# Optimization experiments

Measured on AMD Instinct MI355X. Metric: run time of the kernel, lower is better.

Reference implementation:

```python
import jax, jax.numpy as jnp
import numpy as np

H = 16        # num_heads
NB = 64       # n_buckets
NH = 6        # n_hyperplanes = log2(NB)


def setup_inputs() -> dict:
    key = jax.random.key(0)
    k = jax.random.split(key, 6)
    E = 1024
    B, S = 2, 2048
    return {
        "x": jax.random.normal(k[0], (B, S, E), jnp.float32),
        "Wq": jax.random.normal(k[1], (E, E), jnp.float32) * (E ** -0.5),
        "bq": jax.random.normal(k[2], (E,), jnp.float32) * 0.02,
        "Wv": jax.random.normal(k[3], (E, E), jnp.float32) * (E ** -0.5),
        "bv": jax.random.normal(k[4], (E,), jnp.float32) * 0.02,
        "hyperplanes": jax.random.normal(k[5], (E // H + 1, NH), jnp.float32),
    }


def reference(x, Wq, bq, Wv, bv, hyperplanes):
    B, S, E = x.shape
    Dh = E // H
    # projections (torch Linear: x @ W.T + b)
    q = (x @ Wq.T + bq).reshape(B, S, H, Dh)
    v = (x @ Wv.T + bv).reshape(B, S, H, Dh)

    # LSH buckets from q: append a ones column, sign-project onto hyperplanes
    qa = jnp.concatenate([q, jnp.ones((B, S, H, 1), q.dtype)], axis=-1)  # [B,S,H,Dh+1]
    proj = jnp.einsum('bshe,en->bshn', qa, hyperplanes)
    bits = (proj >= 0).astype(jnp.int32)
    buckets = jnp.einsum('bshn,n->bsh', bits, 2 ** jnp.arange(NH, dtype=jnp.int32))  # [B,S,H]
    b_hs = buckets.transpose(0, 2, 1)  # [B,H,S]

    q = q.transpose(0, 2, 1, 3)  # [B,H,S,Dh]
    v = v.transpose(0, 2, 1, 3)

    # The original sums, over all NB buckets i, of (q with bucket-i tokens zeroed)
    # times its transpose. Closed form of that sum:
    #   sum_i (1-d[bs,i])(1-d[bt,i]) = NB - 2 + [bs == bt]
    scores = jnp.einsum('bhsd,bhtd->bhst', q, q) / jnp.sqrt(jnp.float32(E))
    same = (b_hs[:, :, :, None] == b_hs[:, :, None, :]).astype(scores.dtype)
    coeff = (NB - 2) + same
    attn = jax.nn.softmax(scores * coeff, axis=-1)  # [B,H,S,S]

    out = jnp.einsum('bhst,bhtd->bhsd', attn, v)
    return out.transpose(0, 2, 1, 3).reshape(B, S, E)
```

## Files before the change

### kernel.cpp

```cpp
#include <hip/hip_runtime.h>


typedef short short8 __attribute__((ext_vector_type(8)));
typedef float f32x4 __attribute__((ext_vector_type(4)));
typedef unsigned short us4 __attribute__((ext_vector_type(4)));

__device__ __forceinline__ float bff(unsigned short h) {
    return __uint_as_float(((unsigned int)h) << 16);
}
__device__ __forceinline__ unsigned short f2bf(float f) {
    unsigned int u = __float_as_uint(f);
    u += 0x7fffu + ((u >> 16) & 1u);
    return (unsigned short)(u >> 16);
}

__device__ __forceinline__ void glds16(const unsigned short* g, unsigned short* l) {
    __builtin_amdgcn_global_load_lds(
        (const __attribute__((address_space(1))) unsigned int*)g,
        (__attribute__((address_space(3))) unsigned int*)l, 16, 0, 0);
}

__global__ __launch_bounds__(256) void split_kernel(
    const float* __restrict__ in, unsigned short* __restrict__ hi,
    unsigned short* __restrict__ lo, int n4)
{
    const int idx = blockIdx.x * 256 + threadIdx.x;
    if (idx >= n4) return;
    const float4 v = ((const float4*)in)[idx];
    us4 h;
    h.x = f2bf(v.x); h.y = f2bf(v.y); h.z = f2bf(v.z); h.w = f2bf(v.w);
    ((us4*)hi)[idx] = h;
    if (lo) {
        us4 l;
        l.x = f2bf(v.x - bff(h.x)); l.y = f2bf(v.y - bff(h.y));
        l.z = f2bf(v.z - bff(h.z)); l.w = f2bf(v.w - bff(h.w));
        ((us4*)lo)[idx] = l;
    }
}

__global__ __launch_bounds__(256, 1) void gemm_q(
    const unsigned short* __restrict__ xh, const unsigned short* __restrict__ xl,
    const unsigned short* __restrict__ wh, const unsigned short* __restrict__ wl,
    const float* __restrict__ bias, float* __restrict__ Qf,
    unsigned short* __restrict__ Qb, unsigned short* __restrict__ Qlo)
{
    __shared__ unsigned short Ah[128 * 64], Al[128 * 64];
    __shared__ unsigned short Bh[128 * 64], Bl[128 * 64];

    const int tid = threadIdx.x;
    const int w = tid >> 6, lane = tid & 63;
    const int i = lane & 15, qd = lane >> 4;
    const int l8 = lane >> 3, j = lane & 7;
    const int m0 = blockIdx.x * 128;
    const int n0 = blockIdx.y * 128;
    const int nw = w * 32;

    f32x4 acc[8][2];
#pragma unroll
    for (int a = 0; a < 8; ++a)
#pragma unroll
        for (int b2 = 0; b2 < 2; ++b2) acc[a][b2] = f32x4{0.f, 0.f, 0.f, 0.f};

    for (int k0 = 0; k0 < 1024; k0 += 64) {
        __syncthreads();
        const int gro = ((j ^ l8) << 3);
#pragma unroll
        for (int c = 0; c < 4; ++c) {
            const int r = w * 32 + c * 8;
            const size_t gx = (size_t)(m0 + r + l8) * 1024 + k0 + gro;
            const size_t gw = (size_t)(n0 + r + l8) * 1024 + k0 + gro;
            glds16(xh + gx, &Ah[r * 64]);
            glds16(xl + gx, &Al[r * 64]);
            glds16(wh + gw, &Bh[r * 64]);
            glds16(wl + gw, &Bl[r * 64]);
        }
        __syncthreads();

#pragma unroll
        for (int kc = 0; kc < 2; ++kc) {
            const int ch = (((kc * 4 + qd) ^ (i & 7)) << 3);
            short8 ah[8], al[8], bh2[2], bl2[2];
#pragma unroll
            for (int mm = 0; mm < 8; ++mm) {
                ah[mm] = *(const short8*)&Ah[(mm * 16 + i) * 64 + ch];
                al[mm] = *(const short8*)&Al[(mm * 16 + i) * 64 + ch];
            }
#pragma unroll
            for (int nn = 0; nn < 2; ++nn) {
                bh2[nn] = *(const short8*)&Bh[(nw + nn * 16 + i) * 64 + ch];
                bl2[nn] = *(const short8*)&Bl[(nw + nn * 16 + i) * 64 + ch];
            }
#pragma unroll
            for (int mm = 0; mm < 8; ++mm)
#pragma unroll
                for (int nn = 0; nn < 2; ++nn) {
                    acc[mm][nn] = __builtin_amdgcn_mfma_f32_16x16x32_bf16(
                        ah[mm], bh2[nn], acc[mm][nn], 0, 0, 0);
                    acc[mm][nn] = __builtin_amdgcn_mfma_f32_16x16x32_bf16(
                        al[mm], bh2[nn], acc[mm][nn], 0, 0, 0);
                    acc[mm][nn] = __builtin_amdgcn_mfma_f32_16x16x32_bf16(
                        ah[mm], bl2[nn], acc[mm][nn], 0, 0, 0);
                }
        }
    }

#pragma unroll
    for (int mm = 0; mm < 8; ++mm)
#pragma unroll
        for (int nn = 0; nn < 2; ++nn)
#pragma unroll
            for (int rr = 0; rr < 4; ++rr) {
                const int row = m0 + mm * 16 + qd * 4 + rr;
                const int col = n0 + nw + nn * 16 + i;
                const float v = acc[mm][nn][rr] + bias[col];
                Qf[(size_t)row * 1024 + col] = v;
                const unsigned short hs = f2bf(v);
                const float lo = v - bff(hs);
                const int b = row >> 11, s = row & 2047;
                const int hh = col >> 6, d = col & 63;
                const size_t oi = ((size_t)((b << 4) + hh) * 2048 + s) * 64 + d;
                Qb[oi] = hs;
                Qlo[oi] = f2bf(lo);
            }
}

__global__ __launch_bounds__(256, 1) void gemm_v(
    const unsigned short* __restrict__ wh, const unsigned short* __restrict__ xh,
    const float* __restrict__ bias, unsigned short* __restrict__ Vt)
{
    __shared__ unsigned short Ah[128 * 64];
    __shared__ unsigned short Bh[128 * 64];

    const int tid = threadIdx.x;
    const int w = tid >> 6, lane = tid & 63;
    const int i = lane & 15, qd = lane >> 4;
    const int l8 = lane >> 3, j = lane & 7;
    const int m0 = blockIdx.x * 128;
    const int n0 = blockIdx.y * 128;
    const int nw = w * 32;

    f32x4 acc[8][2];
#pragma unroll
    for (int a = 0; a < 8; ++a)
#pragma unroll
        for (int b2 = 0; b2 < 2; ++b2) acc[a][b2] = f32x4{0.f, 0.f, 0.f, 0.f};

    for (int k0 = 0; k0 < 1024; k0 += 64) {
        __syncthreads();
        const int gro = ((j ^ l8) << 3);
#pragma unroll
        for (int c = 0; c < 4; ++c) {
            const int r = w * 32 + c * 8;
            glds16(wh + (size_t)(m0 + r + l8) * 1024 + k0 + gro, &Ah[r * 64]);
            glds16(xh + (size_t)(n0 + r + l8) * 1024 + k0 + gro, &Bh[r * 64]);
        }
        __syncthreads();

#pragma unroll
        for (int kc = 0; kc < 2; ++kc) {
            const int ch = (((kc * 4 + qd) ^ (i & 7)) << 3);
            short8 af[8], bf2[2];
#pragma unroll
            for (int mm = 0; mm < 8; ++mm)
                af[mm] = *(const short8*)&Ah[(mm * 16 + i) * 64 + ch];
#pragma unroll
            for (int nn = 0; nn < 2; ++nn)
                bf2[nn] = *(const short8*)&Bh[(nw + nn * 16 + i) * 64 + ch];
#pragma unroll
            for (int mm = 0; mm < 8; ++mm)
#pragma unroll
                for (int nn = 0; nn < 2; ++nn)
                    acc[mm][nn] = __builtin_amdgcn_mfma_f32_16x16x32_bf16(
                        af[mm], bf2[nn], acc[mm][nn], 0, 0, 0);
        }
    }

#pragma unroll
    for (int mm = 0; mm < 8; ++mm)
#pragma unroll
        for (int nn = 0; nn < 2; ++nn)
#pragma unroll
            for (int rr = 0; rr < 4; ++rr) {
                const int rch = m0 + mm * 16 + qd * 4 + rr;
                const int tok = n0 + nw + nn * 16 + i;
                const float v = acc[mm][nn][rr] + bias[rch];
                const int b = tok >> 11, s = tok & 2047;
                Vt[((size_t)(b * 1024 + rch)) * 2048 + s] = f2bf(v);
            }
}

__global__ __launch_bounds__(256) void bucket_kernel(
    const float* __restrict__ Qf, const float* __restrict__ hp,
    int* __restrict__ buckets, float* __restrict__ rown)
{
    __shared__ float hpl[65 * 6];
    const int tid = threadIdx.x;
    if (tid < 65 * 6) hpl[tid] = hp[tid];
    __syncthreads();

    const int idx = blockIdx.x * 256 + tid;
    const int m = idx >> 4, h = idx & 15;
    const float* qrow = Qf + (size_t)m * 1024 + h * 64;

    float pj[6];
    float nrm = 0.f;
#pragma unroll
    for (int n = 0; n < 6; ++n) pj[n] = hpl[64 * 6 + n];
    for (int d = 0; d < 64; ++d) {
        const float qv = qrow[d];
        nrm = fmaf(qv, qv, nrm);
#pragma unroll
        for (int n = 0; n < 6; ++n) pj[n] = fmaf(qv, hpl[d * 6 + n], pj[n]);
    }
    int bkt = 0;
#pragma unroll
    for (int n = 0; n < 6; ++n) bkt |= (pj[n] >= 0.f) << n;
    const int off = ((m >> 11) * 16 + h) * 2048 + (m & 2047);
    buckets[off] = bkt;
    rown[off] = nrm;
}

__global__ __launch_bounds__(256, 2) void attn_kernel(
    const unsigned short* __restrict__ Qb, const unsigned short* __restrict__ Qlo,
    const unsigned short* __restrict__ Vt, const int* __restrict__ bks,
    const float* __restrict__ rown, float* __restrict__ out)
{
    __shared__ unsigned short Khi[64 * 64];
    __shared__ unsigned short Klo[64 * 64];
    __shared__ unsigned short Vs[64 * 64];
    __shared__ unsigned short P[4][2][16 * 64];
    __shared__ float smax[4];

    const int tid = threadIdx.x;
    const int w = tid >> 6, lane = tid & 63;
    const int i = lane & 15, qd = lane >> 4;
    const int l8 = lane >> 3, j = lane & 7;
    const int bh = blockIdx.x;
    const int qbase = blockIdx.y * 128 + w * 32;

    const unsigned short* Qh = Qb + (size_t)bh * 2048 * 64;
    const unsigned short* Ql = Qlo + (size_t)bh * 2048 * 64;
    const unsigned short* Vb = Vt + (size_t)bh * 64 * 2048;
    const int* bk = bks + bh * 2048;
    const float* rnh = rown + bh * 2048;

    float lm = 0.f;
    for (int t = tid; t < 2048; t += 256) lm = fmaxf(lm, rnh[t]);
#pragma unroll
    for (int msk = 1; msk < 64; msk <<= 1) lm = fmaxf(lm, __shfl_xor(lm, msk));
    if (lane == 0) smax[w] = lm;
    __syncthreads();
    const float sqM = sqrtf(fmaxf(fmaxf(smax[0], smax[1]),
                                  fmaxf(smax[2], smax[3])));

    float mrow[2][4], lrun[2][4];
    int qbr[2][4];
#pragma unroll
    for (int ms = 0; ms < 2; ++ms)
#pragma unroll
        for (int r = 0; r < 4; ++r) {
            const int row = qbase + ms * 16 + qd * 4 + r;
            mrow[ms][r] = 1.96875f * sqrtf(rnh[row]) * sqM + 0.5f;
            qbr[ms][r] = bk[row];
            lrun[ms][r] = 0.f;
        }

    short8 aqh0[2], aqh1[2], aql0[2], aql1[2];
#pragma unroll
    for (int ms = 0; ms < 2; ++ms) {
        const unsigned short* qp = Qh + (size_t)(qbase + ms * 16 + i) * 64 + qd * 8;
        const unsigned short* lp = Ql + (size_t)(qbase + ms * 16 + i) * 64 + qd * 8;
        aqh0[ms] = *(const short8*)qp; aqh1[ms] = *(const short8*)(qp + 32);
        aql0[ms] = *(const short8*)lp; aql1[ms] = *(const short8*)(lp + 32);
    }

    f32x4 o[2][4];
#pragma unroll
    for (int ms = 0; ms < 2; ++ms)
#pragma unroll
        for (int d = 0; d < 4; ++d) o[ms][d] = f32x4{0.f, 0.f, 0.f, 0.f};

    for (int t0 = 0; t0 < 2048; t0 += 64) {
        __syncthreads();
#pragma unroll
        for (int c2 = 0; c2 < 2; ++c2) {
            const int r = w * 16 + c2 * 8 + l8;
            const int swz = ((j ^ l8) << 3);
            glds16(Qh + (size_t)(t0 + r) * 64 + swz, &Khi[w * 1024 + c2 * 512]);
            glds16(Ql + (size_t)(t0 + r) * 64 + swz, &Klo[w * 1024 + c2 * 512]);
            glds16(Vb + (size_t)r * 2048 + t0 + swz, &Vs[w * 1024 + c2 * 512]);
        }
        __syncthreads();

        f32x4 s[2][4];
        int kb[4];
#pragma unroll
        for (int sub = 0; sub < 4; ++sub) {
            const int kr = sub * 16 + i;
            const int sw = i & 7;
            const short8 bh0 = *(const short8*)&Khi[kr * 64 + ((qd ^ sw) << 3)];
            const short8 bh1 = *(const short8*)&Khi[kr * 64 + (((qd + 4) ^ sw) << 3)];
            const short8 bl0 = *(const short8*)&Klo[kr * 64 + ((qd ^ sw) << 3)];
            const short8 bl1 = *(const short8*)&Klo[kr * 64 + (((qd + 4) ^ sw) << 3)];
            kb[sub] = bk[t0 + kr];
#pragma unroll
            for (int ms = 0; ms < 2; ++ms) {
                f32x4 t = f32x4{0.f, 0.f, 0.f, 0.f};
                t = __builtin_amdgcn_mfma_f32_16x16x32_bf16(aqh0[ms], bh0, t, 0, 0, 0);
                t = __builtin_amdgcn_mfma_f32_16x16x32_bf16(aqh1[ms], bh1, t, 0, 0, 0);
                t = __builtin_amdgcn_mfma_f32_16x16x32_bf16(aql0[ms], bh0, t, 0, 0, 0);
                t = __builtin_amdgcn_mfma_f32_16x16x32_bf16(aql1[ms], bh1, t, 0, 0, 0);
                t = __builtin_amdgcn_mfma_f32_16x16x32_bf16(aqh0[ms], bl0, t, 0, 0, 0);
                t = __builtin_amdgcn_mfma_f32_16x16x32_bf16(aqh1[ms], bl1, t, 0, 0, 0);
                s[ms][sub] = t;
            }
        }

        short8 vb0[4], vb1[4];
#pragma unroll
        for (int dsub = 0; dsub < 4; ++dsub) {
            const int dr = dsub * 16 + i;
            const int sw = i & 7;
            vb0[dsub] = *(const short8*)&Vs[dr * 64 + ((qd ^ sw) << 3)];
            vb1[dsub] = *(const short8*)&Vs[dr * 64 + (((qd + 4) ^ sw) << 3)];
        }

#pragma unroll
        for (int ms = 0; ms < 2; ++ms) {
            unsigned short* Pw = &P[w][ms][0];
#pragma unroll
            for (int sub = 0; sub < 4; ++sub)
#pragma unroll
                for (int r = 0; r < 4; ++r) {
                    const float c = (kb[sub] == qbr[ms][r]) ? 1.96875f : 1.9375f;
                    const float p = __expf(fmaf(s[ms][sub][r], c, -mrow[ms][r]));
                    lrun[ms][r] += p;
                    const int row = qd * 4 + r, col = sub * 16 + i;
                    Pw[row * 64 + (((col >> 3) ^ (row & 7)) << 3) + (col & 7)] =
                        f2bf(p);
                }
            const short8 pa0 = *(const short8*)&Pw[i * 64 + ((qd ^ (i & 7)) << 3)];
            const short8 pa1 = *(const short8*)&Pw[i * 64 + (((qd + 4) ^ (i & 7)) << 3)];
#pragma unroll
            for (int dsub = 0; dsub < 4; ++dsub) {
                o[ms][dsub] = __builtin_amdgcn_mfma_f32_16x16x32_bf16(
                    pa0, vb0[dsub], o[ms][dsub], 0, 0, 0);
                o[ms][dsub] = __builtin_amdgcn_mfma_f32_16x16x32_bf16(
                    pa1, vb1[dsub], o[ms][dsub], 0, 0, 0);
            }
        }
    }

#pragma unroll
    for (int ms = 0; ms < 2; ++ms)
#pragma unroll
        for (int r = 0; r < 4; ++r) {
#pragma unroll
            for (int msk = 1; msk < 16; msk <<= 1)
                lrun[ms][r] += __shfl_xor(lrun[ms][r], msk);
        }
    const int b = bh >> 4, h = bh & 15;
#pragma unroll
    for (int ms = 0; ms < 2; ++ms)
#pragma unroll
        for (int dsub = 0; dsub < 4; ++dsub)
#pragma unroll
            for (int r = 0; r < 4; ++r) {
                const float v = o[ms][dsub][r] / lrun[ms][r];
                const int srow = qbase + ms * 16 + qd * 4 + r;
                out[((size_t)(b * 2048 + srow)) * 1024 + h * 64 + dsub * 16 + i] = v;
            }
}

extern "C" void kernel_launch(void* const* d_in, const int* in_sizes, int n_in,
                              void* d_out, int out_size, void* d_ws, size_t ws_size,
                              hipStream_t stream)
{
    const float* x  = (const float*)d_in[0];
    const float* Wq = (const float*)d_in[1];
    const float* bq = (const float*)d_in[2];
    const float* Wv = (const float*)d_in[3];
    const float* bv = (const float*)d_in[4];
    const float* hp = (const float*)d_in[5];
    float* out = (float*)d_out;

    char* ws = (char*)d_ws;
    const size_t MB = (size_t)1 << 20;
    unsigned short* xh  = (unsigned short*)(ws);
    unsigned short* xl  = (unsigned short*)(ws + 8 * MB);
    unsigned short* Wqh = (unsigned short*)(ws + 16 * MB);
    unsigned short* Wql = (unsigned short*)(ws + 18 * MB);
    unsigned short* Wvh = (unsigned short*)(ws + 20 * MB);
    unsigned short* Qb  = (unsigned short*)(ws + 22 * MB);
    unsigned short* Qlo = (unsigned short*)(ws + 30 * MB);
    unsigned short* Vt  = (unsigned short*)(ws + 38 * MB);
    float*          Qf  = (float*)(ws + 46 * MB);
    int*        buckets = (int*)(ws + 62 * MB);
    float*         rown = (float*)(ws + 62 * MB + 256 * 1024);

    split_kernel<<<dim3(4096), 256, 0, stream>>>(x, xh, xl, 1048576);
    split_kernel<<<dim3(1024), 256, 0, stream>>>(Wq, Wqh, Wql, 262144);
    split_kernel<<<dim3(1024), 256, 0, stream>>>(Wv, Wvh, nullptr, 262144);

    gemm_q<<<dim3(32, 8), 256, 0, stream>>>(xh, xl, Wqh, Wql, bq, Qf, Qb, Qlo);
    gemm_v<<<dim3(8, 32), 256, 0, stream>>>(Wvh, xh, bv, Vt);
    bucket_kernel<<<dim3(256), 256, 0, stream>>>(Qf, hp, buckets, rown);
    attn_kernel<<<dim3(32, 16), 256, 0, stream>>>(Qb, Qlo, Vt, buckets, rown, out);
}
```

Measured before the change: 235.8 us.

## Merge Q/V GEMMs into one launch and shrink attention tiles for occupancy

The Q and V projection GEMMs now run as a single 512-block launch, which removes one kernel launch and lets the V blocks fill CUs left idle by the Q GEMM. The attention kernel drops from 32 to 16 query rows per wave, doubles the grid and raises launch bounds to 4 blocks per CU, aiming for more occupancy and latency hiding. In exchange, each K/V tile loaded into LDS is reused across fewer queries. P is now rounded to bf16 by truncation instead of round-to-nearest, with the row sum built from the truncated values so it stays consistent with what the MFMA consumes.

```diff
diff --git a/kernel.cpp b/kernel.cpp
--- a/kernel.cpp
+++ b/kernel.cpp
@@ -38,11 +38,13 @@
     }
 }
 
-__global__ __launch_bounds__(256, 1) void gemm_q(
+__global__ __launch_bounds__(256, 1) void gemm_qv(
     const unsigned short* __restrict__ xh, const unsigned short* __restrict__ xl,
-    const unsigned short* __restrict__ wh, const unsigned short* __restrict__ wl,
-    const float* __restrict__ bias, float* __restrict__ Qf,
-    unsigned short* __restrict__ Qb, unsigned short* __restrict__ Qlo)
+    const unsigned short* __restrict__ wqh, const unsigned short* __restrict__ wql,
+    const unsigned short* __restrict__ wvh,
+    const float* __restrict__ bq, const float* __restrict__ bv,
+    float* __restrict__ Qf, unsigned short* __restrict__ Qb,
+    unsigned short* __restrict__ Qlo, unsigned short* __restrict__ Vt)
 {
     __shared__ unsigned short Ah[128 * 64], Al[128 * 64];
     __shared__ unsigned short Bh[128 * 64], Bl[128 * 64];
@@ -51,9 +53,9 @@
     const int w = tid >> 6, lane = tid & 63;
     const int i = lane & 15, qd = lane >> 4;
     const int l8 = lane >> 3, j = lane & 7;
-    const int m0 = blockIdx.x * 128;
-    const int n0 = blockIdx.y * 128;
     const int nw = w * 32;
+    const int blk = blockIdx.x;
+    const bool isq = blk < 256;
 
     f32x4 acc[8][2];
 #pragma unroll
@@ -61,132 +63,113 @@
 #pragma unroll
         for (int b2 = 0; b2 < 2; ++b2) acc[a][b2] = f32x4{0.f, 0.f, 0.f, 0.f};
 
-    for (int k0 = 0; k0 < 1024; k0 += 64) {
-        __syncthreads();
-        const int gro = ((j ^ l8) << 3);
-#pragma unroll
-        for (int c = 0; c < 4; ++c) {
-            const int r = w * 32 + c * 8;
-            const size_t gx = (size_t)(m0 + r + l8) * 1024 + k0 + gro;
-            const size_t gw = (size_t)(n0 + r + l8) * 1024 + k0 + gro;
-            glds16(xh + gx, &Ah[r * 64]);
-            glds16(xl + gx, &Al[r * 64]);
-            glds16(wh + gw, &Bh[r * 64]);
-            glds16(wl + gw, &Bl[r * 64]);
-        }
-        __syncthreads();
-
-#pragma unroll
-        for (int kc = 0; kc < 2; ++kc) {
-            const int ch = (((kc * 4 + qd) ^ (i & 7)) << 3);
-            short8 ah[8], al[8], bh2[2], bl2[2];
-#pragma unroll
-            for (int mm = 0; mm < 8; ++mm) {
-                ah[mm] = *(const short8*)&Ah[(mm * 16 + i) * 64 + ch];
-                al[mm] = *(const short8*)&Al[(mm * 16 + i) * 64 + ch];
-            }
-#pragma unroll
-            for (int nn = 0; nn < 2; ++nn) {
-                bh2[nn] = *(const short8*)&Bh[(nw + nn * 16 + i) * 64 + ch];
-                bl2[nn] = *(const short8*)&Bl[(nw + nn * 16 + i) * 64 + ch];
-            }
-#pragma unroll
-            for (int mm = 0; mm < 8; ++mm)
+    const int gro = ((j ^ l8) << 3);
+
+    if (isq) {
+        const int m0 = (blk >> 3) * 128;
+        const int n0 = (blk & 7) * 128;
+        for (int k0 = 0; k0 < 1024; k0 += 64) {
+            __syncthreads();
+#pragma unroll
+            for (int c = 0; c < 4; ++c) {
+                const int r = w * 32 + c * 8;
+                const size_t gx = (size_t)(m0 + r + l8) * 1024 + k0 + gro;
+                const size_t gw = (size_t)(n0 + r + l8) * 1024 + k0 + gro;
+                glds16(xh + gx, &Ah[r * 64]);
+                glds16(xl + gx, &Al[r * 64]);
+                glds16(wqh + gw, &Bh[r * 64]);
+                glds16(wql + gw, &Bl[r * 64]);
+            }
+            __syncthreads();
+#pragma unroll
+            for (int kc = 0; kc < 2; ++kc) {
+                const int ch = (((kc * 4 + qd) ^ (i & 7)) << 3);
+                short8 ah[8], al[8], bh2[2], bl2[2];
+#pragma unroll
+                for (int mm = 0; mm < 8; ++mm) {
+                    ah[mm] = *(const short8*)&Ah[(mm * 16 + i) * 64 + ch];
+                    al[mm] = *(const short8*)&Al[(mm * 16 + i) * 64 + ch];
+                }
 #pragma unroll
                 for (int nn = 0; nn < 2; ++nn) {
-                    acc[mm][nn] = __builtin_amdgcn_mfma_f32_16x16x32_bf16(
-                        ah[mm], bh2[nn], acc[mm][nn], 0, 0, 0);
-                    acc[mm][nn] = __builtin_amdgcn_mfma_f32_16x16x32_bf16(
-                        al[mm], bh2[nn], acc[mm][nn], 0, 0, 0);
-                    acc[mm][nn] = __builtin_amdgcn_mfma_f32_16x16x32_bf16(
-                        ah[mm], bl2[nn], acc[mm][nn], 0, 0, 0);
+                    bh2[nn] = *(const short8*)&Bh[(nw + nn * 16 + i) * 64 + ch];
+                    bl2[nn] = *(const short8*)&Bl[(nw + nn * 16 + i) * 64 + ch];
                 }
-        }
-    }
-
-#pragma unroll
-    for (int mm = 0; mm < 8; ++mm)
-#pragma unroll
-        for (int nn = 0; nn < 2; ++nn)
-#pragma unroll
-            for (int rr = 0; rr < 4; ++rr) {
-                const int row = m0 + mm * 16 + qd * 4 + rr;
-                const int col = n0 + nw + nn * 16 + i;
-                const float v = acc[mm][nn][rr] + bias[col];
-                Qf[(size_t)row * 1024 + col] = v;
-                const unsigned short hs = f2bf(v);
-                const float lo = v - bff(hs);
-                const int b = row >> 11, s = row & 2047;
-                const int hh = col >> 6, d = col & 63;
-                const size_t oi = ((size_t)((b << 4) + hh) * 2048 + s) * 64 + d;
-                Qb[oi] = hs;
-                Qlo[oi] = f2bf(lo);
-            }
-}
-
-__global__ __launch_bounds__(256, 1) void gemm_v(
-    const unsigned short* __restrict__ wh, const unsigned short* __restrict__ xh,
-    const float* __restrict__ bias, unsigned short* __restrict__ Vt)
-{
-    __shared__ unsigned short Ah[128 * 64];
-    __shared__ unsigned short Bh[128 * 64];
-
-    const int tid = threadIdx.x;
-    const int w = tid >> 6, lane = tid & 63;
-    const int i = lane & 15, qd = lane >> 4;
-    const int l8 = lane >> 3, j = lane & 7;
-    const int m0 = blockIdx.x * 128;
-    const int n0 = blockIdx.y * 128;
-    const int nw = w * 32;
-
-    f32x4 acc[8][2];
-#pragma unroll
-    for (int a = 0; a < 8; ++a)
-#pragma unroll
-        for (int b2 = 0; b2 < 2; ++b2) acc[a][b2] = f32x4{0.f, 0.f, 0.f, 0.f};
-
-    for (int k0 = 0; k0 < 1024; k0 += 64) {
-        __syncthreads();
-        const int gro = ((j ^ l8) << 3);
-#pragma unroll
-        for (int c = 0; c < 4; ++c) {
-            const int r = w * 32 + c * 8;
-            glds16(wh + (size_t)(m0 + r + l8) * 1024 + k0 + gro, &Ah[r * 64]);
-            glds16(xh + (size_t)(n0 + r + l8) * 1024 + k0 + gro, &Bh[r * 64]);
-        }
-        __syncthreads();
-
-#pragma unroll
-        for (int kc = 0; kc < 2; ++kc) {
-            const int ch = (((kc * 4 + qd) ^ (i & 7)) << 3);
-            short8 af[8], bf2[2];
-#pragma unroll
-            for (int mm = 0; mm < 8; ++mm)
-                af[mm] = *(const short8*)&Ah[(mm * 16 + i) * 64 + ch];
+#pragma unroll
+                for (int mm = 0; mm < 8; ++mm)
+#pragma unroll
+                    for (int nn = 0; nn < 2; ++nn) {
+                        acc[mm][nn] = __builtin_amdgcn_mfma_f32_16x16x32_bf16(
+                            ah[mm], bh2[nn], acc[mm][nn], 0, 0, 0);
+                        acc[mm][nn] = __builtin_amdgcn_mfma_f32_16x16x32_bf16(
+                            al[mm], bh2[nn], acc[mm][nn], 0, 0, 0);
+                        acc[mm][nn] = __builtin_amdgcn_mfma_f32_16x16x32_bf16(
+                            ah[mm], bl2[nn], acc[mm][nn], 0, 0, 0);
+                    }
+            }
+        }
+#pragma unroll
+        for (int mm = 0; mm < 8; ++mm)
 #pragma unroll
             for (int nn = 0; nn < 2; ++nn)
-                bf2[nn] = *(const short8*)&Bh[(nw + nn * 16 + i) * 64 + ch];
-#pragma unroll
-            for (int mm = 0; mm < 8; ++mm)
+#pragma unroll
+                for (int rr = 0; rr < 4; ++rr) {
+                    const int row = m0 + mm * 16 + qd * 4 + rr;
+                    const int col = n0 + nw + nn * 16 + i;
+                    const float v = acc[mm][nn][rr] + bq[col];
+                    Qf[(size_t)row * 1024 + col] = v;
+                    const unsigned short hs = f2bf(v);
+                    const float lo = v - bff(hs);
+                    const int b = row >> 11, s = row & 2047;
+                    const int hh = col >> 6, d = col & 63;
+                    const size_t oi = ((size_t)((b << 4) + hh) * 2048 + s) * 64 + d;
+                    Qb[oi] = hs;
+                    Qlo[oi] = f2bf(lo);
+                }
+    } else {
+        const int b2 = blk - 256;
+        const int m0 = (b2 & 7) * 128;
+        const int n0 = (b2 >> 3) * 128;
+        for (int k0 = 0; k0 < 1024; k0 += 64) {
+            __syncthreads();
+#pragma unroll
+            for (int c = 0; c < 4; ++c) {
+                const int r = w * 32 + c * 8;
+                glds16(wvh + (size_t)(m0 + r + l8) * 1024 + k0 + gro, &Ah[r * 64]);
+                glds16(xh + (size_t)(n0 + r + l8) * 1024 + k0 + gro, &Bh[r * 64]);
+            }
+            __syncthreads();
+#pragma unroll
+            for (int kc = 0; kc < 2; ++kc) {
+                const int ch = (((kc * 4 + qd) ^ (i & 7)) << 3);
+                short8 af[8], bf2[2];
+#pragma unroll
+                for (int mm = 0; mm < 8; ++mm)
+                    af[mm] = *(const short8*)&Ah[(mm * 16 + i) * 64 + ch];
 #pragma unroll
                 for (int nn = 0; nn < 2; ++nn)
-                    acc[mm][nn] = __builtin_amdgcn_mfma_f32_16x16x32_bf16(
-                        af[mm], bf2[nn], acc[mm][nn], 0, 0, 0);
-        }
-    }
-
-#pragma unroll
-    for (int mm = 0; mm < 8; ++mm)
-#pragma unroll
-        for (int nn = 0; nn < 2; ++nn)
-#pragma unroll
-            for (int rr = 0; rr < 4; ++rr) {
-                const int rch = m0 + mm * 16 + qd * 4 + rr;
-                const int tok = n0 + nw + nn * 16 + i;
-                const float v = acc[mm][nn][rr] + bias[rch];
-                const int b = tok >> 11, s = tok & 2047;
-                Vt[((size_t)(b * 1024 + rch)) * 2048 + s] = f2bf(v);
-            }
+                    bf2[nn] = *(const short8*)&Bh[(nw + nn * 16 + i) * 64 + ch];
+#pragma unroll
+                for (int mm = 0; mm < 8; ++mm)
+#pragma unroll
+                    for (int nn = 0; nn < 2; ++nn)
+                        acc[mm][nn] = __builtin_amdgcn_mfma_f32_16x16x32_bf16(
+                            af[mm], bf2[nn], acc[mm][nn], 0, 0, 0);
+            }
+        }
+#pragma unroll
+        for (int mm = 0; mm < 8; ++mm)
+#pragma unroll
+            for (int nn = 0; nn < 2; ++nn)
+#pragma unroll
+                for (int rr = 0; rr < 4; ++rr) {
+                    const int rch = m0 + mm * 16 + qd * 4 + rr;
+                    const int tok = n0 + nw + nn * 16 + i;
+                    const float v = acc[mm][nn][rr] + bv[rch];
+                    const int b = tok >> 11, s = tok & 2047;
+                    Vt[((size_t)(b * 1024 + rch)) * 2048 + s] = f2bf(v);
+                }
+    }
 }
 
 __global__ __launch_bounds__(256) void bucket_kernel(
@@ -220,7 +203,7 @@
     rown[off] = nrm;
 }
 
-__global__ __launch_bounds__(256, 2) void attn_kernel(
+__global__ __launch_bounds__(256, 4) void attn_kernel(
     const unsigned short* __restrict__ Qb, const unsigned short* __restrict__ Qlo,
     const unsigned short* __restrict__ Vt, const int* __restrict__ bks,
     const float* __restrict__ rown, float* __restrict__ out)
@@ -228,7 +211,7 @@
     __shared__ unsigned short Khi[64 * 64];
     __shared__ unsigned short Klo[64 * 64];
     __shared__ unsigned short Vs[64 * 64];
-    __shared__ unsigned short P[4][2][16 * 64];
+    __shared__ unsigned short P[4][16 * 64];
     __shared__ float smax[4];
 
     const int tid = threadIdx.x;
@@ -236,13 +219,14 @@
     const int i = lane & 15, qd = lane >> 4;
     const int l8 = lane >> 3, j = lane & 7;
     const int bh = blockIdx.x;
-    const int qbase = blockIdx.y * 128 + w * 32;
+    const int q0 = blockIdx.y * 64 + w * 16;
 
     const unsigned short* Qh = Qb + (size_t)bh * 2048 * 64;
     const unsigned short* Ql = Qlo + (size_t)bh * 2048 * 64;
     const unsigned short* Vb = Vt + (size_t)bh * 64 * 2048;
     const int* bk = bks + bh * 2048;
     const float* rnh = rown + bh * 2048;
+    unsigned short* Pw = &P[w][0];
 
     float lm = 0.f;
     for (int t = tid; t < 2048; t += 256) lm = fmaxf(lm, rnh[t]);
@@ -253,32 +237,24 @@
     const float sqM = sqrtf(fmaxf(fmaxf(smax[0], smax[1]),
                                   fmaxf(smax[2], smax[3])));
 
-    float mrow[2][4], lrun[2][4];
-    int qbr[2][4];
-#pragma unroll
-    for (int ms = 0; ms < 2; ++ms)
-#pragma unroll
-        for (int r = 0; r < 4; ++r) {
-            const int row = qbase + ms * 16 + qd * 4 + r;
-            mrow[ms][r] = 1.96875f * sqrtf(rnh[row]) * sqM + 0.5f;
-            qbr[ms][r] = bk[row];
-            lrun[ms][r] = 0.f;
-        }
-
-    short8 aqh0[2], aqh1[2], aql0[2], aql1[2];
-#pragma unroll
-    for (int ms = 0; ms < 2; ++ms) {
-        const unsigned short* qp = Qh + (size_t)(qbase + ms * 16 + i) * 64 + qd * 8;
-        const unsigned short* lp = Ql + (size_t)(qbase + ms * 16 + i) * 64 + qd * 8;
-        aqh0[ms] = *(const short8*)qp; aqh1[ms] = *(const short8*)(qp + 32);
-        aql0[ms] = *(const short8*)lp; aql1[ms] = *(const short8*)(lp + 32);
-    }
-
-    f32x4 o[2][4];
-#pragma unroll
-    for (int ms = 0; ms < 2; ++ms)
-#pragma unroll
-        for (int d = 0; d < 4; ++d) o[ms][d] = f32x4{0.f, 0.f, 0.f, 0.f};
+    float mrow[4], lrun[4];
+    int qbr[4];
+#pragma unroll
+    for (int r = 0; r < 4; ++r) {
+        const int row = q0 + qd * 4 + r;
+        mrow[r] = 1.96875f * sqrtf(rnh[row]) * sqM + 0.5f;
+        qbr[r] = bk[row];
+        lrun[r] = 0.f;
+    }
+
+    const unsigned short* qp = Qh + (size_t)(q0 + i) * 64 + qd * 8;
+    const unsigned short* lp = Ql + (size_t)(q0 + i) * 64 + qd * 8;
+    const short8 aqh0 = *(const short8*)qp, aqh1 = *(const short8*)(qp + 32);
+    const short8 aql0 = *(const short8*)lp, aql1 = *(const short8*)(lp + 32);
+
+    f32x4 o[4];
+#pragma unroll
+    for (int d = 0; d < 4; ++d) o[d] = f32x4{0.f, 0.f, 0.f, 0.f};
 
     for (int t0 = 0; t0 < 2048; t0 += 64) {
         __syncthreads();
@@ -292,7 +268,7 @@
         }
         __syncthreads();
 
-        f32x4 s[2][4];
+        f32x4 s[4];
         int kb[4];
 #pragma unroll
         for (int sub = 0; sub < 4; ++sub) {
@@ -303,17 +279,14 @@
             const short8 bl0 = *(const short8*)&Klo[kr * 64 + ((qd ^ sw) << 3)];
             const short8 bl1 = *(const short8*)&Klo[kr * 64 + (((qd + 4) ^ sw) << 3)];
             kb[sub] = bk[t0 + kr];
-#pragma unroll
-            for (int ms = 0; ms < 2; ++ms) {
-                f32x4 t = f32x4{0.f, 0.f, 0.f, 0.f};
-                t = __builtin_amdgcn_mfma_f32_16x16x32_bf16(aqh0[ms], bh0, t, 0, 0, 0);
-                t = __builtin_amdgcn_mfma_f32_16x16x32_bf16(aqh1[ms], bh1, t, 0, 0, 0);
-                t = __builtin_amdgcn_mfma_f32_16x16x32_bf16(aql0[ms], bh0, t, 0, 0, 0);
-                t = __builtin_amdgcn_mfma_f32_16x16x32_bf16(aql1[ms], bh1, t, 0, 0, 0);
-                t = __builtin_amdgcn_mfma_f32_16x16x32_bf16(aqh0[ms], bl0, t, 0, 0, 0);
-                t = __builtin_amdgcn_mfma_f32_16x16x32_bf16(aqh1[ms], bl1, t, 0, 0, 0);
-                s[ms][sub] = t;
-            }
+            f32x4 t = f32x4{0.f, 0.f, 0.f, 0.f};
+            t = __builtin_amdgcn_mfma_f32_16x16x32_bf16(aqh0, bh0, t, 0, 0, 0);
+            t = __builtin_amdgcn_mfma_f32_16x16x32_bf16(aqh1, bh1, t, 0, 0, 0);
+            t = __builtin_amdgcn_mfma_f32_16x16x32_bf16(aql0, bh0, t, 0, 0, 0);
+            t = __builtin_amdgcn_mfma_f32_16x16x32_bf16(aql1, bh1, t, 0, 0, 0);
+            t = __builtin_amdgcn_mfma_f32_16x16x32_bf16(aqh0, bl0, t, 0, 0, 0);
+            t = __builtin_amdgcn_mfma_f32_16x16x32_bf16(aqh1, bl1, t, 0, 0, 0);
+            s[sub] = t;
         }
 
         short8 vb0[4], vb1[4];
@@ -326,50 +299,42 @@
         }
 
 #pragma unroll
-        for (int ms = 0; ms < 2; ++ms) {
-            unsigned short* Pw = &P[w][ms][0];
-#pragma unroll
-            for (int sub = 0; sub < 4; ++sub)
-#pragma unroll
-                for (int r = 0; r < 4; ++r) {
-                    const float c = (kb[sub] == qbr[ms][r]) ? 1.96875f : 1.9375f;
-                    const float p = __expf(fmaf(s[ms][sub][r], c, -mrow[ms][r]));
-                    lrun[ms][r] += p;
-                    const int row = qd * 4 + r, col = sub * 16 + i;
-                    Pw[row * 64 + (((col >> 3) ^ (row & 7)) << 3) + (col & 7)] =
-                        f2bf(p);
-                }
-            const short8 pa0 = *(const short8*)&Pw[i * 64 + ((qd ^ (i & 7)) << 3)];
-            const short8 pa1 = *(const short8*)&Pw[i * 64 + (((qd + 4) ^ (i & 7)) << 3)];
-#pragma unroll
-            for (int dsub = 0; dsub < 4; ++dsub) {
-                o[ms][dsub] = __builtin_amdgcn_mfma_f32_16x16x32_bf16(
-                    pa0, vb0[dsub], o[ms][dsub], 0, 0, 0);
-                o[ms][dsub] = __builtin_amdgcn_mfma_f32_16x16x32_bf16(
-                    pa1, vb1[dsub], o[ms][dsub], 0, 0, 0);
-            }
-        }
-    }
-
-#pragma unroll
-    for (int ms = 0; ms < 2; ++ms)
+        for (int sub = 0; sub < 4; ++sub)
+#pragma unroll
+            for (int r = 0; r < 4; ++r) {
+                const float c = (kb[sub] == qbr[r]) ? 1.96875f : 1.9375f;
+                const float p = __expf(fmaf(s[sub][r], c, -mrow[r]));
+                const unsigned int pu = __float_as_uint(p);
+                lrun[r] += __uint_as_float(pu & 0xffff0000u);
+                const int row = qd * 4 + r, col = sub * 16 + i;
+                Pw[row * 64 + (((col >> 3) ^ (row & 7)) << 3) + (col & 7)] =
+                    (unsigned short)(pu >> 16);
+            }
+        const short8 pa0 = *(const short8*)&Pw[i * 64 + ((qd ^ (i & 7)) << 3)];
+        const short8 pa1 = *(const short8*)&Pw[i * 64 + (((qd + 4) ^ (i & 7)) << 3)];
+
+#pragma unroll
+        for (int dsub = 0; dsub < 4; ++dsub) {
+            o[dsub] = __builtin_amdgcn_mfma_f32_16x16x32_bf16(pa0, vb0[dsub], o[dsub], 0, 0, 0);
+            o[dsub] = __builtin_amdgcn_mfma_f32_16x16x32_bf16(pa1, vb1[dsub], o[dsub], 0, 0, 0);
+        }
+    }
+
+#pragma unroll
+    for (int r = 0; r < 4; ++r) {
+#pragma unroll
+        for (int msk = 1; msk < 16; msk <<= 1)
+            lrun[r] += __shfl_xor(lrun[r], msk);
+    }
+    const int b = bh >> 4, h = bh & 15;
+#pragma unroll
+    for (int dsub = 0; dsub < 4; ++dsub)
 #pragma unroll
         for (int r = 0; r < 4; ++r) {
-#pragma unroll
-            for (int msk = 1; msk < 16; msk <<= 1)
-                lrun[ms][r] += __shfl_xor(lrun[ms][r], msk);
-        }
-    const int b = bh >> 4, h = bh & 15;
-#pragma unroll
-    for (int ms = 0; ms < 2; ++ms)
-#pragma unroll
-        for (int dsub = 0; dsub < 4; ++dsub)
-#pragma unroll
-            for (int r = 0; r < 4; ++r) {
-                const float v = o[ms][dsub][r] / lrun[ms][r];
-                const int srow = qbase + ms * 16 + qd * 4 + r;
-                out[((size_t)(b * 2048 + srow)) * 1024 + h * 64 + dsub * 16 + i] = v;
-            }
+            const float v = o[dsub][r] / lrun[r];
+            const int srow = q0 + qd * 4 + r;
+            out[((size_t)(b * 2048 + srow)) * 1024 + h * 64 + dsub * 16 + i] = v;
+        }
 }
 
 extern "C" void kernel_launch(void* const* d_in, const int* in_sizes, int n_in,
@@ -402,8 +367,8 @@
     split_kernel<<<dim3(1024), 256, 0, stream>>>(Wq, Wqh, Wql, 262144);
     split_kernel<<<dim3(1024), 256, 0, stream>>>(Wv, Wvh, nullptr, 262144);
 
-    gemm_q<<<dim3(32, 8), 256, 0, stream>>>(xh, xl, Wqh, Wql, bq, Qf, Qb, Qlo);
-    gemm_v<<<dim3(8, 32), 256, 0, stream>>>(Wvh, xh, bv, Vt);
+    gemm_qv<<<dim3(512), 256, 0, stream>>>(xh, xl, Wqh, Wql, Wvh, bq, bv,
+                                           Qf, Qb, Qlo, Vt);
     bucket_kernel<<<dim3(256), 256, 0, stream>>>(Qf, hp, buckets, rown);
-    attn_kernel<<<dim3(32, 16), 256, 0, stream>>>(Qb, Qlo, Vt, buckets, rown, out);
-}
+    attn_kernel<<<dim3(32, 32), 256, 0, stream>>>(Qb, Qlo, Vt, buckets, rown, out);
+}
```

New measurement: 235.5 us. Within noise of the previous version (-0.1%).

## Merge Q/V GEMMs, split attention over key halves, add combine kernel

Applied to the files above, without the earlier changes.

Merges the Q and V projection GEMMs into one launch of 512 blocks so both fill the GPU together. Splits the attention key range into two halves via a z grid dimension, which doubles the block count and raises the occupancy hint from 2 to 4. Each half writes unnormalized numerators and row sums, and a new combine kernel adds them and normalizes. It also switches to exp2 with prescaled constants, sums the bf16-truncated probabilities instead of rounded ones, vectorizes the bucket kernel loads, and halves the P shared buffer. The extra combine pass adds global memory traffic, and the partial outputs reuse workspace regions (xh/xl, Qf) that are no longer needed by then.

```diff
diff --git a/kernel.cpp b/kernel.cpp
--- a/kernel.cpp
+++ b/kernel.cpp
@@ -38,11 +38,13 @@
     }
 }
 
-__global__ __launch_bounds__(256, 1) void gemm_q(
+__global__ __launch_bounds__(256, 1) void gemm_qv(
     const unsigned short* __restrict__ xh, const unsigned short* __restrict__ xl,
-    const unsigned short* __restrict__ wh, const unsigned short* __restrict__ wl,
-    const float* __restrict__ bias, float* __restrict__ Qf,
-    unsigned short* __restrict__ Qb, unsigned short* __restrict__ Qlo)
+    const unsigned short* __restrict__ wqh, const unsigned short* __restrict__ wql,
+    const unsigned short* __restrict__ wvh,
+    const float* __restrict__ bq, const float* __restrict__ bv,
+    float* __restrict__ Qf, unsigned short* __restrict__ Qb,
+    unsigned short* __restrict__ Qlo, unsigned short* __restrict__ Vt)
 {
     __shared__ unsigned short Ah[128 * 64], Al[128 * 64];
     __shared__ unsigned short Bh[128 * 64], Bl[128 * 64];
@@ -51,9 +53,9 @@
     const int w = tid >> 6, lane = tid & 63;
     const int i = lane & 15, qd = lane >> 4;
     const int l8 = lane >> 3, j = lane & 7;
-    const int m0 = blockIdx.x * 128;
-    const int n0 = blockIdx.y * 128;
     const int nw = w * 32;
+    const int blk = blockIdx.x;
+    const bool isq = blk < 256;
 
     f32x4 acc[8][2];
 #pragma unroll
@@ -61,132 +63,113 @@
 #pragma unroll
         for (int b2 = 0; b2 < 2; ++b2) acc[a][b2] = f32x4{0.f, 0.f, 0.f, 0.f};
 
-    for (int k0 = 0; k0 < 1024; k0 += 64) {
-        __syncthreads();
-        const int gro = ((j ^ l8) << 3);
-#pragma unroll
-        for (int c = 0; c < 4; ++c) {
-            const int r = w * 32 + c * 8;
-            const size_t gx = (size_t)(m0 + r + l8) * 1024 + k0 + gro;
-            const size_t gw = (size_t)(n0 + r + l8) * 1024 + k0 + gro;
-            glds16(xh + gx, &Ah[r * 64]);
-            glds16(xl + gx, &Al[r * 64]);
-            glds16(wh + gw, &Bh[r * 64]);
-            glds16(wl + gw, &Bl[r * 64]);
-        }
-        __syncthreads();
-
-#pragma unroll
-        for (int kc = 0; kc < 2; ++kc) {
-            const int ch = (((kc * 4 + qd) ^ (i & 7)) << 3);
-            short8 ah[8], al[8], bh2[2], bl2[2];
-#pragma unroll
-            for (int mm = 0; mm < 8; ++mm) {
-                ah[mm] = *(const short8*)&Ah[(mm * 16 + i) * 64 + ch];
-                al[mm] = *(const short8*)&Al[(mm * 16 + i) * 64 + ch];
-            }
-#pragma unroll
-            for (int nn = 0; nn < 2; ++nn) {
-                bh2[nn] = *(const short8*)&Bh[(nw + nn * 16 + i) * 64 + ch];
-                bl2[nn] = *(const short8*)&Bl[(nw + nn * 16 + i) * 64 + ch];
-            }
-#pragma unroll
-            for (int mm = 0; mm < 8; ++mm)
+    const int gro = ((j ^ l8) << 3);
+
+    if (isq) {
+        const int m0 = (blk >> 3) * 128;
+        const int n0 = (blk & 7) * 128;
+        for (int k0 = 0; k0 < 1024; k0 += 64) {
+            __syncthreads();
+#pragma unroll
+            for (int c = 0; c < 4; ++c) {
+                const int r = w * 32 + c * 8;
+                const size_t gx = (size_t)(m0 + r + l8) * 1024 + k0 + gro;
+                const size_t gw = (size_t)(n0 + r + l8) * 1024 + k0 + gro;
+                glds16(xh + gx, &Ah[r * 64]);
+                glds16(xl + gx, &Al[r * 64]);
+                glds16(wqh + gw, &Bh[r * 64]);
+                glds16(wql + gw, &Bl[r * 64]);
+            }
+            __syncthreads();
+#pragma unroll
+            for (int kc = 0; kc < 2; ++kc) {
+                const int ch = (((kc * 4 + qd) ^ (i & 7)) << 3);
+                short8 ah[8], al[8], bh2[2], bl2[2];
+#pragma unroll
+                for (int mm = 0; mm < 8; ++mm) {
+                    ah[mm] = *(const short8*)&Ah[(mm * 16 + i) * 64 + ch];
+                    al[mm] = *(const short8*)&Al[(mm * 16 + i) * 64 + ch];
+                }
 #pragma unroll
                 for (int nn = 0; nn < 2; ++nn) {
-                    acc[mm][nn] = __builtin_amdgcn_mfma_f32_16x16x32_bf16(
-                        ah[mm], bh2[nn], acc[mm][nn], 0, 0, 0);
-                    acc[mm][nn] = __builtin_amdgcn_mfma_f32_16x16x32_bf16(
-                        al[mm], bh2[nn], acc[mm][nn], 0, 0, 0);
-                    acc[mm][nn] = __builtin_amdgcn_mfma_f32_16x16x32_bf16(
-                        ah[mm], bl2[nn], acc[mm][nn], 0, 0, 0);
+                    bh2[nn] = *(const short8*)&Bh[(nw + nn * 16 + i) * 64 + ch];
+                    bl2[nn] = *(const short8*)&Bl[(nw + nn * 16 + i) * 64 + ch];
                 }
-        }
-    }
-
-#pragma unroll
-    for (int mm = 0; mm < 8; ++mm)
-#pragma unroll
-        for (int nn = 0; nn < 2; ++nn)
-#pragma unroll
-            for (int rr = 0; rr < 4; ++rr) {
-                const int row = m0 + mm * 16 + qd * 4 + rr;
-                const int col = n0 + nw + nn * 16 + i;
-                const float v = acc[mm][nn][rr] + bias[col];
-                Qf[(size_t)row * 1024 + col] = v;
-                const unsigned short hs = f2bf(v);
-                const float lo = v - bff(hs);
-                const int b = row >> 11, s = row & 2047;
-                const int hh = col >> 6, d = col & 63;
-                const size_t oi = ((size_t)((b << 4) + hh) * 2048 + s) * 64 + d;
-                Qb[oi] = hs;
-                Qlo[oi] = f2bf(lo);
-            }
-}
-
-__global__ __launch_bounds__(256, 1) void gemm_v(
-    const unsigned short* __restrict__ wh, const unsigned short* __restrict__ xh,
-    const float* __restrict__ bias, unsigned short* __restrict__ Vt)
-{
-    __shared__ unsigned short Ah[128 * 64];
-    __shared__ unsigned short Bh[128 * 64];
-
-    const int tid = threadIdx.x;
-    const int w = tid >> 6, lane = tid & 63;
-    const int i = lane & 15, qd = lane >> 4;
-    const int l8 = lane >> 3, j = lane & 7;
-    const int m0 = blockIdx.x * 128;
-    const int n0 = blockIdx.y * 128;
-    const int nw = w * 32;
-
-    f32x4 acc[8][2];
-#pragma unroll
-    for (int a = 0; a < 8; ++a)
-#pragma unroll
-        for (int b2 = 0; b2 < 2; ++b2) acc[a][b2] = f32x4{0.f, 0.f, 0.f, 0.f};
-
-    for (int k0 = 0; k0 < 1024; k0 += 64) {
-        __syncthreads();
-        const int gro = ((j ^ l8) << 3);
-#pragma unroll
-        for (int c = 0; c < 4; ++c) {
-            const int r = w * 32 + c * 8;
-            glds16(wh + (size_t)(m0 + r + l8) * 1024 + k0 + gro, &Ah[r * 64]);
-            glds16(xh + (size_t)(n0 + r + l8) * 1024 + k0 + gro, &Bh[r * 64]);
-        }
-        __syncthreads();
-
-#pragma unroll
-        for (int kc = 0; kc < 2; ++kc) {
-            const int ch = (((kc * 4 + qd) ^ (i & 7)) << 3);
-            short8 af[8], bf2[2];
-#pragma unroll
-            for (int mm = 0; mm < 8; ++mm)
-                af[mm] = *(const short8*)&Ah[(mm * 16 + i) * 64 + ch];
+#pragma unroll
+                for (int mm = 0; mm < 8; ++mm)
+#pragma unroll
+                    for (int nn = 0; nn < 2; ++nn) {
+                        acc[mm][nn] = __builtin_amdgcn_mfma_f32_16x16x32_bf16(
+                            ah[mm], bh2[nn], acc[mm][nn], 0, 0, 0);
+                        acc[mm][nn] = __builtin_amdgcn_mfma_f32_16x16x32_bf16(
+                            al[mm], bh2[nn], acc[mm][nn], 0, 0, 0);
+                        acc[mm][nn] = __builtin_amdgcn_mfma_f32_16x16x32_bf16(
+                            ah[mm], bl2[nn], acc[mm][nn], 0, 0, 0);
+                    }
+            }
+        }
+#pragma unroll
+        for (int mm = 0; mm < 8; ++mm)
 #pragma unroll
             for (int nn = 0; nn < 2; ++nn)
-                bf2[nn] = *(const short8*)&Bh[(nw + nn * 16 + i) * 64 + ch];
-#pragma unroll
-            for (int mm = 0; mm < 8; ++mm)
+#pragma unroll
+                for (int rr = 0; rr < 4; ++rr) {
+                    const int row = m0 + mm * 16 + qd * 4 + rr;
+                    const int col = n0 + nw + nn * 16 + i;
+                    const float v = acc[mm][nn][rr] + bq[col];
+                    Qf[(size_t)row * 1024 + col] = v;
+                    const unsigned short hs = f2bf(v);
+                    const float lo = v - bff(hs);
+                    const int b = row >> 11, s = row & 2047;
+                    const int hh = col >> 6, d = col & 63;
+                    const size_t oi = ((size_t)((b << 4) + hh) * 2048 + s) * 64 + d;
+                    Qb[oi] = hs;
+                    Qlo[oi] = f2bf(lo);
+                }
+    } else {
+        const int b2 = blk - 256;
+        const int m0 = (b2 & 7) * 128;
+        const int n0 = (b2 >> 3) * 128;
+        for (int k0 = 0; k0 < 1024; k0 += 64) {
+            __syncthreads();
+#pragma unroll
+            for (int c = 0; c < 4; ++c) {
+                const int r = w * 32 + c * 8;
+                glds16(wvh + (size_t)(m0 + r + l8) * 1024 + k0 + gro, &Ah[r * 64]);
+                glds16(xh + (size_t)(n0 + r + l8) * 1024 + k0 + gro, &Bh[r * 64]);
+            }
+            __syncthreads();
+#pragma unroll
+            for (int kc = 0; kc < 2; ++kc) {
+                const int ch = (((kc * 4 + qd) ^ (i & 7)) << 3);
+                short8 af[8], bf2[2];
+#pragma unroll
+                for (int mm = 0; mm < 8; ++mm)
+                    af[mm] = *(const short8*)&Ah[(mm * 16 + i) * 64 + ch];
 #pragma unroll
                 for (int nn = 0; nn < 2; ++nn)
-                    acc[mm][nn] = __builtin_amdgcn_mfma_f32_16x16x32_bf16(
-                        af[mm], bf2[nn], acc[mm][nn], 0, 0, 0);
-        }
-    }
-
-#pragma unroll
-    for (int mm = 0; mm < 8; ++mm)
-#pragma unroll
-        for (int nn = 0; nn < 2; ++nn)
-#pragma unroll
-            for (int rr = 0; rr < 4; ++rr) {
-                const int rch = m0 + mm * 16 + qd * 4 + rr;
-                const int tok = n0 + nw + nn * 16 + i;
-                const float v = acc[mm][nn][rr] + bias[rch];
-                const int b = tok >> 11, s = tok & 2047;
-                Vt[((size_t)(b * 1024 + rch)) * 2048 + s] = f2bf(v);
-            }
+                    bf2[nn] = *(const short8*)&Bh[(nw + nn * 16 + i) * 64 + ch];
+#pragma unroll
+                for (int mm = 0; mm < 8; ++mm)
+#pragma unroll
+                    for (int nn = 0; nn < 2; ++nn)
+                        acc[mm][nn] = __builtin_amdgcn_mfma_f32_16x16x32_bf16(
+                            af[mm], bf2[nn], acc[mm][nn], 0, 0, 0);
+            }
+        }
+#pragma unroll
+        for (int mm = 0; mm < 8; ++mm)
+#pragma unroll
+            for (int nn = 0; nn < 2; ++nn)
+#pragma unroll
+                for (int rr = 0; rr < 4; ++rr) {
+                    const int rch = m0 + mm * 16 + qd * 4 + rr;
+                    const int tok = n0 + nw + nn * 16 + i;
+                    const float v = acc[mm][nn][rr] + bv[rch];
+                    const int b = tok >> 11, s = tok & 2047;
+                    Vt[((size_t)(b * 1024 + rch)) * 2048 + s] = f2bf(v);
+                }
+    }
 }
 
 __global__ __launch_bounds__(256) void bucket_kernel(
@@ -200,17 +183,23 @@
 
     const int idx = blockIdx.x * 256 + tid;
     const int m = idx >> 4, h = idx & 15;
-    const float* qrow = Qf + (size_t)m * 1024 + h * 64;
+    const float4* q4 = (const float4*)(Qf + (size_t)m * 1024 + h * 64);
 
     float pj[6];
     float nrm = 0.f;
 #pragma unroll
     for (int n = 0; n < 6; ++n) pj[n] = hpl[64 * 6 + n];
-    for (int d = 0; d < 64; ++d) {
-        const float qv = qrow[d];
-        nrm = fmaf(qv, qv, nrm);
-#pragma unroll
-        for (int n = 0; n < 6; ++n) pj[n] = fmaf(qv, hpl[d * 6 + n], pj[n]);
+    for (int d4 = 0; d4 < 16; ++d4) {
+        const float4 qv = q4[d4];
+        nrm = fmaf(qv.x, qv.x, nrm); nrm = fmaf(qv.y, qv.y, nrm);
+        nrm = fmaf(qv.z, qv.z, nrm); nrm = fmaf(qv.w, qv.w, nrm);
+#pragma unroll
+        for (int n = 0; n < 6; ++n) {
+            pj[n] = fmaf(qv.x, hpl[(d4 * 4 + 0) * 6 + n], pj[n]);
+            pj[n] = fmaf(qv.y, hpl[(d4 * 4 + 1) * 6 + n], pj[n]);
+            pj[n] = fmaf(qv.z, hpl[(d4 * 4 + 2) * 6 + n], pj[n]);
+            pj[n] = fmaf(qv.w, hpl[(d4 * 4 + 3) * 6 + n], pj[n]);
+        }
     }
     int bkt = 0;
 #pragma unroll
@@ -220,15 +209,17 @@
     rown[off] = nrm;
 }
 
-__global__ __launch_bounds__(256, 2) void attn_kernel(
+__global__ __launch_bounds__(256, 4) void attn_kernel(
     const unsigned short* __restrict__ Qb, const unsigned short* __restrict__ Qlo,
     const unsigned short* __restrict__ Vt, const int* __restrict__ bks,
-    const float* __restrict__ rown, float* __restrict__ out)
+    const float* __restrict__ rown,
+    float* __restrict__ onum0, float* __restrict__ onum1,
+    float* __restrict__ lsum)
 {
     __shared__ unsigned short Khi[64 * 64];
     __shared__ unsigned short Klo[64 * 64];
     __shared__ unsigned short Vs[64 * 64];
-    __shared__ unsigned short P[4][2][16 * 64];
+    __shared__ unsigned short P[4][16 * 64];
     __shared__ float smax[4];
 
     const int tid = threadIdx.x;
@@ -237,12 +228,15 @@
     const int l8 = lane >> 3, j = lane & 7;
     const int bh = blockIdx.x;
     const int qbase = blockIdx.y * 128 + w * 32;
+    const int kh = blockIdx.z;
 
     const unsigned short* Qh = Qb + (size_t)bh * 2048 * 64;
     const unsigned short* Ql = Qlo + (size_t)bh * 2048 * 64;
     const unsigned short* Vb = Vt + (size_t)bh * 64 * 2048;
     const int* bk = bks + bh * 2048;
     const float* rnh = rown + bh * 2048;
+    float* onum = kh ? onum1 : onum0;
+    unsigned short* Pw = &P[w][0];
 
     float lm = 0.f;
     for (int t = tid; t < 2048; t += 256) lm = fmaxf(lm, rnh[t]);
@@ -253,14 +247,14 @@
     const float sqM = sqrtf(fmaxf(fmaxf(smax[0], smax[1]),
                                   fmaxf(smax[2], smax[3])));
 
-    float mrow[2][4], lrun[2][4];
+    float m2row[2][4], lrun[2][4];
     int qbr[2][4];
 #pragma unroll
     for (int ms = 0; ms < 2; ++ms)
 #pragma unroll
         for (int r = 0; r < 4; ++r) {
             const int row = qbase + ms * 16 + qd * 4 + r;
-            mrow[ms][r] = 1.96875f * sqrtf(rnh[row]) * sqM + 0.5f;
+            m2row[ms][r] = 2.84030586f * sqrtf(rnh[row]) * sqM + 0.72134754f;
             qbr[ms][r] = bk[row];
             lrun[ms][r] = 0.f;
         }
@@ -280,7 +274,8 @@
 #pragma unroll
         for (int d = 0; d < 4; ++d) o[ms][d] = f32x4{0.f, 0.f, 0.f, 0.f};
 
-    for (int t0 = 0; t0 < 2048; t0 += 64) {
+    const int tlo = kh * 1024, thi = tlo + 1024;
+    for (int t0 = tlo; t0 < thi; t0 += 64) {
         __syncthreads();
 #pragma unroll
         for (int c2 = 0; c2 < 2; ++c2) {
@@ -327,17 +322,18 @@
 
 #pragma unroll
         for (int ms = 0; ms < 2; ++ms) {
-            unsigned short* Pw = &P[w][ms][0];
 #pragma unroll
             for (int sub = 0; sub < 4; ++sub)
 #pragma unroll
                 for (int r = 0; r < 4; ++r) {
-                    const float c = (kb[sub] == qbr[ms][r]) ? 1.96875f : 1.9375f;
-                    const float p = __expf(fmaf(s[ms][sub][r], c, -mrow[ms][r]));
-                    lrun[ms][r] += p;
+                    const float c2f = (kb[sub] == qbr[ms][r]) ? 2.84030586f
+                                                              : 2.79522164f;
+                    const float p = exp2f(fmaf(s[ms][sub][r], c2f, -m2row[ms][r]));
+                    const unsigned int pu = __float_as_uint(p);
+                    lrun[ms][r] += __uint_as_float(pu & 0xffff0000u);
                     const int row = qd * 4 + r, col = sub * 16 + i;
                     Pw[row * 64 + (((col >> 3) ^ (row & 7)) << 3) + (col & 7)] =
-                        f2bf(p);
+                        (unsigned short)(pu >> 16);
                 }
             const short8 pa0 = *(const short8*)&Pw[i * 64 + ((qd ^ (i & 7)) << 3)];
             const short8 pa1 = *(const short8*)&Pw[i * 64 + (((qd + 4) ^ (i & 7)) << 3)];
@@ -361,15 +357,44 @@
         }
     const int b = bh >> 4, h = bh & 15;
 #pragma unroll
-    for (int ms = 0; ms < 2; ++ms)
+    for (int ms = 0; ms < 2; ++ms) {
+        if (i == 0) {
+#pragma unroll
+            for (int r = 0; r < 4; ++r) {
+                const int srow = qbase + ms * 16 + qd * 4 + r;
+                lsum[(size_t)kh * 65536 + bh * 2048 + srow] = lrun[ms][r];
+            }
+        }
 #pragma unroll
         for (int dsub = 0; dsub < 4; ++dsub)
 #pragma unroll
             for (int r = 0; r < 4; ++r) {
-                const float v = o[ms][dsub][r] / lrun[ms][r];
                 const int srow = qbase + ms * 16 + qd * 4 + r;
-                out[((size_t)(b * 2048 + srow)) * 1024 + h * 64 + dsub * 16 + i] = v;
-            }
+                onum[((size_t)(b * 2048 + srow)) * 1024 + h * 64 + dsub * 16 + i] =
+                    o[ms][dsub][r];
+            }
+    }
+}
+
+__global__ __launch_bounds__(256) void combine_kernel(
+    const float* __restrict__ onum0, const float* __restrict__ onum1,
+    const float* __restrict__ lsum, float* __restrict__ out)
+{
+    const int t = blockIdx.x * 256 + threadIdx.x;
+    const int row = t >> 8;
+    const int c4 = t & 255;
+    const int h = c4 >> 4;
+    const int bh = (row >> 11) * 16 + h;
+    const int s = row & 2047;
+    const float la = lsum[bh * 2048 + s];
+    const float lb = lsum[65536 + bh * 2048 + s];
+    const float rcp = 1.f / (la + lb);
+    const float4 na = ((const float4*)onum0)[t];
+    const float4 nb = ((const float4*)onum1)[t];
+    float4 o;
+    o.x = (na.x + nb.x) * rcp; o.y = (na.y + nb.y) * rcp;
+    o.z = (na.z + nb.z) * rcp; o.w = (na.w + nb.w) * rcp;
+    ((float4*)out)[t] = o;
 }
 
 extern "C" void kernel_launch(void* const* d_in, const int* in_sizes, int n_in,
@@ -397,13 +422,18 @@
     float*          Qf  = (float*)(ws + 46 * MB);
     int*        buckets = (int*)(ws + 62 * MB);
     float*         rown = (float*)(ws + 62 * MB + 256 * 1024);
+    float*         lsum = (float*)(ws + 62 * MB + 512 * 1024);
+    float* onum0 = (float*)(ws);
+    float* onum1 = (float*)(ws + 46 * MB);
 
     split_kernel<<<dim3(4096), 256, 0, stream>>>(x, xh, xl, 1048576);
     split_kernel<<<dim3(1024), 256, 0, stream>>>(Wq, Wqh, Wql, 262144);
     split_kernel<<<dim3(1024), 256, 0, stream>>>(Wv, Wvh, nullptr, 262144);
 
-    gemm_q<<<dim3(32, 8), 256, 0, stream>>>(xh, xl, Wqh, Wql, bq, Qf, Qb, Qlo);
-    gemm_v<<<dim3(8, 32), 256, 0, stream>>>(Wvh, xh, bv, Vt);
+    gemm_qv<<<dim3(512), 256, 0, stream>>>(xh, xl, Wqh, Wql, Wvh, bq, bv,
+                                           Qf, Qb, Qlo, Vt);
     bucket_kernel<<<dim3(256), 256, 0, stream>>>(Qf, hp, buckets, rown);
-    attn_kernel<<<dim3(32, 16), 256, 0, stream>>>(Qb, Qlo, Vt, buckets, rown, out);
-}
+    attn_kernel<<<dim3(32, 16, 2), 256, 0, stream>>>(Qb, Qlo, Vt, buckets, rown,
+                                                     onum0, onum1, lsum);
+    combine_kernel<<<dim3(4096), 256, 0, stream>>>(onum0, onum1, lsum, out);
+}
```

New measurement: 428.8 us. 81.8% more time.
